# Optimization experiments

Hardware: AMD Instinct MI355X
Metric: run time of the kernel (lower is better)

## Reference

```python
import jax, jax.numpy as jnp
import numpy as np

TOPK = 13
ALPHA = 1.0
BETA = 6.0
NUM_CLASSES = 80
NUM_ANCHORS = 100000
NUM_GT = 512
EPS = 1e-9


def _make_boxes(key, n):
    k1, k2 = jax.random.split(key)
    lt = jax.random.uniform(k1, (n, 2)) * 0.5          # x1, y1 in [0, 0.5)
    wh = jax.random.uniform(k2, (n, 2)) * 0.5 + 1e-3   # positive width/height
    return jnp.concatenate([lt, lt + wh], axis=-1)      # [n, 4] valid xyxy


def setup_inputs() -> dict:
    key = jax.random.key(0)
    k1, k2, k3, k4 = jax.random.split(key, 4)
    pd_scores = jax.random.uniform(k1, (NUM_ANCHORS, NUM_CLASSES), dtype=jnp.float32)
    pd_bboxes = _make_boxes(k2, NUM_ANCHORS)
    gt_labels = jax.random.randint(k3, (NUM_GT, 1), 0, NUM_CLASSES, dtype=jnp.int64)
    gt_bboxes = _make_boxes(k4, NUM_GT)
    return {"pd_scores": pd_scores, "pd_bboxes": pd_bboxes,
            "gt_labels": gt_labels, "gt_bboxes": gt_bboxes}


def box_iou(a, b):
    # a: [G, 4], b: [A, 4] in xyxy -> iou [G, A]
    lt = jnp.maximum(a[:, None, :2], b[None, :, :2])
    rb = jnp.minimum(a[:, None, 2:], b[None, :, 2:])
    wh = jnp.clip(rb - lt, 0.0)
    inter = wh[..., 0] * wh[..., 1]                      # [G, A]
    area_a = (a[:, 2] - a[:, 0]) * (a[:, 3] - a[:, 1])   # [G]
    area_b = (b[:, 2] - b[:, 0]) * (b[:, 3] - b[:, 1])   # [A]
    union = area_a[:, None] + area_b[None, :] - inter
    return inter / (union + EPS)


def select_topk_candidates(metrics, topk):
    # metrics: [G, A] -> bool mask [G, A] of per-row topk entries
    _, topk_idx = jax.lax.top_k(metrics, topk)           # [G, topk]
    rows = jnp.arange(metrics.shape[0])[:, None]
    mask = jnp.zeros(metrics.shape, dtype=bool)
    return mask.at[rows, topk_idx].set(True)


def reference(pd_scores, pd_bboxes, gt_labels, gt_bboxes):
    labels = gt_labels.reshape(-1)                       # [G]
    ious = box_iou(gt_bboxes, pd_bboxes)                 # [G, A]
    scores = pd_scores[:, labels].T                      # [G, A] gather by gt class
    metrics = (scores ** ALPHA) * (ious ** BETA)         # alignment metric [G, A]
    is_in_topk = select_topk_candidates(metrics, TOPK)   # [G, A] bool
    max_metrics = jnp.max(metrics, axis=0)               # [A]
    max_indices = jnp.argmax(metrics, axis=0)            # [A]
    target_labels = labels[max_indices]                  # [A]
    target_labels = jnp.where(max_metrics <= 0, NUM_CLASSES, target_labels)
    target_bboxes = gt_bboxes[max_indices]               # [A, 4]
    # is_in_topk is computed (as in the original) and returned so the topk/scatter
    return target_labels, target_bboxes, max_metrics, is_in_topk
```

## Files before the change

### kernel.cpp

```cpp
#include <hip/hip_runtime.h>
#include <cfloat>
#include <cstdint>

#define AN 100000
#define GN 512
#define NC 80
#define KK 13

#define CHUNKS 8
#define CH_LEN 12544
#define DUMP 16
#define GSLICE 8
#define GPS (GN / GSLICE)

typedef unsigned long long ull;

__device__ __forceinline__ float iou6_f(float4 g, float ga, float4 p)
{
    float pa = (p.z - p.x) * (p.w - p.y);
    float ltx = fmaxf(g.x, p.x), lty = fmaxf(g.y, p.y);
    float rbx = fminf(g.z, p.z), rby = fminf(g.w, p.w);
    float w = fmaxf(rbx - ltx, 0.0f), h = fmaxf(rby - lty, 0.0f);
    float inter = w * h;
    float uni = ga + pa - inter;
    float iou = inter / (uni + 1e-9f);
    float i2 = iou * iou;
    return i2 * i2 * i2;
}

__device__ __forceinline__ unsigned f2ord(float f)
{
    unsigned b = __float_as_uint(f);
    return b ^ (unsigned)(((int)b >> 31) | 0x80000000);
}
__device__ __forceinline__ float ord2f(unsigned u)
{
    unsigned b = (u & 0x80000000u) ? (u ^ 0x80000000u) : ~u;
    return __uint_as_float(b);
}

__device__ __forceinline__ void csw(float& va, int& ia, float& vb, int& ib)
{
    bool sw = (va < vb) || (va == vb && ia > ib);
    float tv = sw ? vb : va; int ti = sw ? ib : ia;
    vb = sw ? va : vb; ib = sw ? ia : ib;
    va = tv; ia = ti;
}

__device__ __forceinline__ void wsync()
{
    __builtin_amdgcn_sched_barrier(0);
    asm volatile("s_waitcnt lgkmcnt(0)" ::: "memory");
    __builtin_amdgcn_sched_barrier(0);
}

__device__ float flush_x(int lane, int n, const float* cand_v, const int* cand_i,
                         float& inc_v, int& inc_i)
{
    wsync();
    float v[8]; int ix[8];
    #pragma unroll
    for (int k = 0; k < 8; ++k) {
        int j = lane + (k << 6);
        bool ok = j < n;
        v[k]  = ok ? cand_v[j] : -FLT_MAX;
        ix[k] = ok ? cand_i[j] : 0x7fffffff;
    }
    csw(v[0],ix[0],v[1],ix[1]); csw(v[2],ix[2],v[3],ix[3]);
    csw(v[4],ix[4],v[5],ix[5]); csw(v[6],ix[6],v[7],ix[7]);
    csw(v[0],ix[0],v[2],ix[2]); csw(v[1],ix[1],v[3],ix[3]);
    csw(v[4],ix[4],v[6],ix[6]); csw(v[5],ix[5],v[7],ix[7]);
    csw(v[1],ix[1],v[2],ix[2]); csw(v[5],ix[5],v[6],ix[6]);
    csw(v[0],ix[0],v[4],ix[4]); csw(v[1],ix[1],v[5],ix[5]);
    csw(v[2],ix[2],v[6],ix[6]); csw(v[3],ix[3],v[7],ix[7]);
    csw(v[2],ix[2],v[4],ix[4]); csw(v[3],ix[3],v[5],ix[5]);
    csw(v[1],ix[1],v[2],ix[2]); csw(v[3],ix[3],v[4],ix[4]);
    csw(v[5],ix[5],v[6],ix[6]);
    bool c[8];
    #pragma unroll
    for (int j = 0; j < 8; ++j)
        c[j] = (v[j] > inc_v) || (v[j] == inc_v && ix[j] < inc_i);
    float h[9]; int hi[9];
    h[0] = c[0] ? v[0] : inc_v;  hi[0] = c[0] ? ix[0] : inc_i;
    #pragma unroll
    for (int j = 1; j < 8; ++j) {
        h[j]  = c[j] ? v[j]  : (c[j-1] ? inc_v : v[j-1]);
        hi[j] = c[j] ? ix[j] : (c[j-1] ? inc_i : ix[j-1]);
    }
    h[8] = c[7] ? inc_v : v[7];  hi[8] = c[7] ? inc_i : ix[7];

    float th = -FLT_MAX;
    #pragma unroll
    for (int r = 0; r < KK; ++r) {
        ull myp = ((ull)f2ord(h[0]) << 32) | (unsigned)(~hi[0]);
        ull p = myp;
        #pragma unroll
        for (int o = 32; o >= 1; o >>= 1) {
            ull q = __shfl_xor(p, o);
            p = p > q ? p : q;
        }
        float wv = ord2f((unsigned)(p >> 32));
        int   wi = (int)~((unsigned)p);
        if (lane == r) { inc_v = wv; inc_i = wi; }
        bool pop = (myp == p);
        #pragma unroll
        for (int j = 0; j < 8; ++j) {
            h[j]  = pop ? h[j+1]  : h[j];
            hi[j] = pop ? hi[j+1] : hi[j];
        }
        h[8]  = pop ? -FLT_MAX   : h[8];
        hi[8] = pop ? 0x7fffffff : hi[8];
        th = wv;
    }
    return th;
}

__device__ __forceinline__ void insert13(float* v, int* ix, float m, int a)
{
    bool worse = (m < v[KK - 1]) || (m == v[KK - 1] && a > ix[KK - 1]);
    if (worse) return;
    int p = 0;
    #pragma unroll
    for (int j = 0; j < KK; ++j)
        p += ((v[j] > m) || (v[j] == m && ix[j] < a)) ? 1 : 0;
    #pragma unroll
    for (int j = KK - 1; j >= 1; --j) {
        bool sh = (j > p);
        v[j]  = sh ? v[j - 1]  : v[j];
        ix[j] = sh ? ix[j - 1] : ix[j];
    }
    #pragma unroll
    for (int j = 0; j < KK; ++j) if (j == p) { v[j] = m; ix[j] = a; }
}

__global__ __launch_bounds__(256) void transpose_scores(
    const float* __restrict__ ps, float* __restrict__ scT)
{
    __shared__ float tile[64][NC + 1];
    int a0 = blockIdx.x * 64;
    int tid = threadIdx.x;
    for (int i = tid; i < 64 * NC / 4; i += 256) {
        int fi = i * 4;
        int a = fi / NC, c = fi % NC;
        if (a0 + a < AN) {
            float4 v = *reinterpret_cast<const float4*>(ps + (size_t)(a0 + a) * NC + c);
            tile[a][c] = v.x; tile[a][c + 1] = v.y; tile[a][c + 2] = v.z; tile[a][c + 3] = v.w;
        }
    }
    __syncthreads();
    int j = tid & 63, cg = tid >> 6;
    int a = a0 + j;
    if (a < AN) {
        for (int c = cg; c < NC; c += 4)
            scT[(size_t)c * AN + a] = tile[j][c];
    }
}

__global__ __launch_bounds__(256) void argmax_part(
    const float* __restrict__ pd_bboxes,
    const int*   __restrict__ gt_labels,
    const float* __restrict__ gt_bboxes,
    const float* __restrict__ scT,
    ull* __restrict__ part)
{
    __shared__ float4 gb[GPS];
    __shared__ float  ga[GPS];
    __shared__ int    glb[GPS];
    int slice = blockIdx.x & (GSLICE - 1);
    int ab = (blockIdx.x >> 3) * 512;
    int tid = threadIdx.x;
    int g0 = slice * GPS;
    if (tid < GPS) {
        float4 bb = ((const float4*)gt_bboxes)[g0 + tid];
        gb[tid] = bb;
        ga[tid] = (bb.z - bb.x) * (bb.w - bb.y);
        glb[tid] = gt_labels[g0 + tid];
    }
    __syncthreads();
    int aa = ab + tid, ab2 = ab + 256 + tid;
    bool okA = aa < AN, okB = ab2 < AN;
    int ca = okA ? aa : AN - 1, cb = okB ? ab2 : AN - 1;
    float4 pba = ((const float4*)pd_bboxes)[ca];
    float4 pbb = ((const float4*)pd_bboxes)[cb];
    float bestA = -1.0f, bestB = -1.0f;
    int bgA = 0, bgB = 0;
    for (int i = 0; i < GPS; ++i) {
        float4 gx = gb[i];
        float gax = ga[i];
        int lab = glb[i];
        const float* srow = scT + (size_t)lab * AN;
        float i6a = iou6_f(gx, gax, pba);
        float i6b = iou6_f(gx, gax, pbb);
        float sa = (i6a > bestA) ? srow[ca] : 0.0f;
        float sb = (i6b > bestB) ? srow[cb] : 0.0f;
        float ma = sa * i6a;
        float mb = sb * i6b;
        if (ma > bestA) { bestA = ma; bgA = i; }
        if (mb > bestB) { bestB = mb; bgB = i; }
    }
    if (okA)
        part[(size_t)slice * AN + aa] =
            ((ull)__float_as_uint(bestA) << 32) | (ull)(0xFFFFFFFFu - (unsigned)(g0 + bgA));
    if (okB)
        part[(size_t)slice * AN + ab2] =
            ((ull)__float_as_uint(bestB) << 32) | (ull)(0xFFFFFFFFu - (unsigned)(g0 + bgB));
}

__global__ __launch_bounds__(256) void argmax_combine(
    const ull* __restrict__ part,
    const int* __restrict__ gt_labels,
    const float* __restrict__ gt_bboxes,
    float* __restrict__ out)
{
    int a = blockIdx.x * 256 + threadIdx.x;
    if (a >= AN) return;
    ull p = part[a];
    #pragma unroll
    for (int s = 1; s < GSLICE; ++s) {
        ull q = part[(size_t)s * AN + a];
        p = p > q ? p : q;
    }
    unsigned g = 0xFFFFFFFFu - (unsigned)(p & 0xFFFFFFFFull);
    float best = __uint_as_float((unsigned)(p >> 32));
    out[a] = (best <= 0.0f) ? (float)NC : (float)gt_labels[g];
    ((float4*)(out + AN))[a] = ((const float4*)gt_bboxes)[g];
    out[(size_t)5 * AN + a] = best;
}

__device__ __forceinline__ void loadT(int tb, int lane,
    const float4* __restrict__ pd4, const float* __restrict__ srow,
    float4& B0, float4& B1, float4& B2, float4& B3,
    float& s0, float& s1, float& s2, float& s3)
{
    int a0 = tb + lane;
    int c0 = min(a0,       AN - 1);
    int c1 = min(a0 + 64,  AN - 1);
    int c2 = min(a0 + 128, AN - 1);
    int c3 = min(a0 + 192, AN - 1);
    B0 = pd4[c0]; B1 = pd4[c1]; B2 = pd4[c2]; B3 = pd4[c3];
    s0 = srow[c0]; s1 = srow[c1]; s2 = srow[c2]; s3 = srow[c3];
}

__device__ __forceinline__ void procT(
    int tb, int aend, int lane, uint64_t lt,
    float4 B0, float4 B1, float4 B2, float4 B3,
    float s0, float s1, float s2, float s3,
    float4 b, float gax, float& th, int& cnt,
    float* cand_v, int* cand_i, float& inc_v, int& inc_i)
{
    int a0 = tb + lane, a1 = a0 + 64, a2 = a0 + 128, a3 = a0 + 192;
    float m0 = s0 * iou6_f(b, gax, B0);
    float m1 = s1 * iou6_f(b, gax, B1);
    float m2 = s2 * iou6_f(b, gax, B2);
    float m3 = s3 * iou6_f(b, gax, B3);
    bool h0 = (m0 > th) && (a0 < aend);
    bool h1 = (m1 > th) && (a1 < aend);
    bool h2 = (m2 > th) && (a2 < aend);
    bool h3 = (m3 > th) && (a3 < aend);
    if (__any(h0 | h1 | h2 | h3)) {
        uint64_t B;
        B = __ballot(h0);
        if (h0) { int p = cnt + __popcll(B & lt); cand_v[p] = m0; cand_i[p] = a0; }
        cnt += __popcll(B);
        B = __ballot(h1);
        if (h1) { int p = cnt + __popcll(B & lt); cand_v[p] = m1; cand_i[p] = a1; }
        cnt += __popcll(B);
        B = __ballot(h2);
        if (h2) { int p = cnt + __popcll(B & lt); cand_v[p] = m2; cand_i[p] = a2; }
        cnt += __popcll(B);
        B = __ballot(h3);
        if (h3) { int p = cnt + __popcll(B & lt); cand_v[p] = m3; cand_i[p] = a3; }
        cnt += __popcll(B);
        if (cnt >= 256) {
            th = flush_x(lane, cnt, cand_v, cand_i, inc_v, inc_i);
            cnt = 0;
        }
    }
}

__global__ __launch_bounds__(256, 4) void topk_pass1(
    const float* __restrict__ pd_bboxes,
    const int*   __restrict__ gt_labels,
    const float* __restrict__ gt_bboxes,
    const float* __restrict__ scT,
    float* __restrict__ out_v, int* __restrict__ out_i)
{
    __shared__ float cvA[4][512];
    __shared__ int   ciA[4][512];
    int w = threadIdx.x >> 6, lane = threadIdx.x & 63;
    float* cand_v = cvA[w]; int* cand_i = ciA[w];
    uint64_t lt = (1ull << lane) - 1ull;
    int gid = blockIdx.x * 4 + w;
    int g = gid & (GN - 1), c = gid >> 9;

    float4 b = ((const float4*)gt_bboxes)[g];
    float gax = (b.z - b.x) * (b.w - b.y);
    int lab = gt_labels[g];
    const float* srow = scT + (size_t)lab * AN;
    const float4* pd4 = (const float4*)pd_bboxes;

    int base = c * CH_LEN;
    int len = min(CH_LEN, AN - base);
    int aend = base + len;
    int NT = (len + 255) >> 8;

    float th = -FLT_MAX; int cnt = 0;
    float inc_v = -FLT_MAX; int inc_i = 0x7fffffff;

    float4 X0, X1, X2, X3, Y0, Y1, Y2, Y3;
    float xs0, xs1, xs2, xs3, ys0, ys1, ys2, ys3;

    loadT(base, lane, pd4, srow, X0, X1, X2, X3, xs0, xs1, xs2, xs3);
    int i = 0, tb = base;
    while (true) {
        if (i + 1 < NT)
            loadT(tb + 256, lane, pd4, srow, Y0, Y1, Y2, Y3, ys0, ys1, ys2, ys3);
        procT(tb, aend, lane, lt, X0, X1, X2, X3, xs0, xs1, xs2, xs3,
              b, gax, th, cnt, cand_v, cand_i, inc_v, inc_i);
        ++i; tb += 256;
        if (i >= NT) break;
        if (i + 1 < NT)
            loadT(tb + 256, lane, pd4, srow, X0, X1, X2, X3, xs0, xs1, xs2, xs3);
        procT(tb, aend, lane, lt, Y0, Y1, Y2, Y3, ys0, ys1, ys2, ys3,
              b, gax, th, cnt, cand_v, cand_i, inc_v, inc_i);
        ++i; tb += 256;
        if (i >= NT) break;
    }

    if (cnt > 0)
        flush_x(lane, cnt, cand_v, cand_i, inc_v, inc_i);

    if (lane < DUMP) {
        size_t o = ((size_t)g * CHUNKS + c) * DUMP + lane;
        out_v[o] = (lane < KK) ? inc_v : -FLT_MAX;
        out_i[o] = (lane < KK) ? inc_i : 0x7fffffff;
    }
}

__global__ __launch_bounds__(256) void topk_finalize(
    const float* __restrict__ in_v, const int* __restrict__ in_i,
    float* __restrict__ mask)
{
    int g = blockIdx.x, tid = threadIdx.x;
    float4* row4 = (float4*)(mask + (size_t)g * AN);
    float4 z = make_float4(0.f, 0.f, 0.f, 0.f);
    for (int j = tid; j < AN / 4; j += 256) row4[j] = z;
    __syncthreads();
    if (tid >= 64) return;
    int lane = tid;
    size_t rb = (size_t)g * (CHUNKS * DUMP);
    float v0 = in_v[rb + lane], v1 = in_v[rb + 64 + lane];
    int   i0 = in_i[rb + lane], i1 = in_i[rb + 64 + lane];
    csw(v0, i0, v1, i1);
    #pragma unroll
    for (int r = 0; r < KK; ++r) {
        ull myp = ((ull)f2ord(v0) << 32) | (unsigned)(~i0);
        ull p = myp;
        #pragma unroll
        for (int o = 32; o >= 1; o >>= 1) {
            ull q = __shfl_xor(p, o);
            p = p > q ? p : q;
        }
        int wi = (int)~((unsigned)p);
        if (lane == r) mask[(size_t)g * AN + wi] = 1.0f;
        bool pop = (myp == p);
        v0 = pop ? v1 : v0;          i0 = pop ? i1 : i0;
        v1 = pop ? -FLT_MAX : v1;    i1 = pop ? 0x7fffffff : i1;
    }
}

__global__ __launch_bounds__(256) void argmax_kernel(
    const float* __restrict__ pd_scores,
    const float* __restrict__ pd_bboxes,
    const int*   __restrict__ gt_labels,
    const float* __restrict__ gt_bboxes,
    const float* __restrict__ scT, int use_t,
    float* __restrict__ out)
{
    __shared__ float4 gb[GN];
    __shared__ float  ga[GN];
    __shared__ int    gl[GN];
    int tid = threadIdx.x;
    for (int g = tid; g < GN; g += 256) {
        float4 b = reinterpret_cast<const float4*>(gt_bboxes)[g];
        gb[g] = b;
        ga[g] = (b.z - b.x) * (b.w - b.y);
        gl[g] = gt_labels[g];
    }
    __syncthreads();
    int a = blockIdx.x * 256 + tid;
    if (a >= AN) return;
    float4 pb = reinterpret_cast<const float4*>(pd_bboxes)[a];
    float best = -1.0f; int bg = 0;
    for (int g = 0; g < GN; ++g) {
        int lab = gl[g];
        float sc = use_t ? scT[(size_t)lab * AN + a] : pd_scores[(size_t)a * NC + lab];
        float m = sc * iou6_f(gb[g], ga[g], pb);
        if (m > best) { best = m; bg = g; }
    }
    out[a] = (best <= 0.0f) ? (float)NC : (float)gl[bg];
    reinterpret_cast<float4*>(out + AN)[a] = gb[bg];
    out[5 * AN + a] = best;
}

__global__ __launch_bounds__(256) void topk_kernel_fallback(
    const float* __restrict__ pd_scores,
    const float* __restrict__ pd_bboxes,
    const int*   __restrict__ gt_labels,
    const float* __restrict__ gt_bboxes,
    const float* __restrict__ scT, int use_t,
    float* __restrict__ mask)
{
    __shared__ float sv[256 * KK];
    __shared__ int   si[256 * KK];
    int g = blockIdx.x, tid = threadIdx.x;
    float4 b = reinterpret_cast<const float4*>(gt_bboxes)[g];
    float gax = (b.z - b.x) * (b.w - b.y);
    int lab = gt_labels[g];
    float v[KK]; int idx[KK];
    #pragma unroll
    for (int j = 0; j < KK; ++j) { v[j] = -FLT_MAX; idx[j] = 0x7fffffff; }
    for (int a = tid; a < AN; a += 256) {
        float4 pb = reinterpret_cast<const float4*>(pd_bboxes)[a];
        float sc = use_t ? scT[(size_t)lab * AN + a] : pd_scores[(size_t)a * NC + lab];
        float m = sc * iou6_f(b, gax, pb);
        insert13(v, idx, m, a);
    }
    #pragma unroll
    for (int j = 0; j < KK; ++j) { sv[tid * KK + j] = v[j]; si[tid * KK + j] = idx[j]; }
    for (int off = 128; off >= 1; off >>= 1) {
        __syncthreads();
        if (tid < off) {
            int i = 0, jj = 0;
            float ov[KK]; int oi[KK];
            #pragma unroll
            for (int t = 0; t < KK; ++t) {
                float va = sv[tid * KK + i];          int ia = si[tid * KK + i];
                float vb = sv[(tid + off) * KK + jj]; int ib = si[(tid + off) * KK + jj];
                bool ta = (va > vb) || (va == vb && ia < ib);
                ov[t] = ta ? va : vb; oi[t] = ta ? ia : ib;
                i += ta ? 1 : 0; jj += ta ? 0 : 1;
            }
            #pragma unroll
            for (int t = 0; t < KK; ++t) { sv[tid * KK + t] = ov[t]; si[tid * KK + t] = oi[t]; }
        }
    }
    __syncthreads();
    if (tid < KK) mask[(size_t)g * AN + si[tid]] = 1.0f;
}

extern "C" void kernel_launch(void* const* d_in, const int* in_sizes, int n_in,
                              void* d_out, int out_size, void* d_ws, size_t ws_size,
                              hipStream_t stream)
{
    const float* pd_scores = (const float*)d_in[0];
    const float* pd_bboxes = (const float*)d_in[1];
    const int*   gt_labels = (const int*)d_in[2];
    const float* gt_bboxes = (const float*)d_in[3];
    float* out  = (float*)d_out;
    float* mask = out + (size_t)6 * AN;

    const size_t scT_b  = (size_t)NC * AN * sizeof(float);
    const size_t auxn   = (size_t)GN * CHUNKS * DUMP;
    const size_t aux_b  = auxn * 8;
    const size_t part_b = (size_t)GSLICE * AN * sizeof(ull);

    float* scT   = (float*)d_ws;
    float* aux_v = (float*)((char*)d_ws + scT_b);
    int*   aux_i = (int*)(aux_v + auxn);
    ull*   part  = (ull*)((char*)d_ws + scT_b + aux_b);

    if (ws_size >= scT_b + aux_b + part_b) {
        transpose_scores<<<(AN + 63) / 64, 256, 0, stream>>>(pd_scores, scT);
        topk_pass1<<<GN * CHUNKS / 4, 256, 0, stream>>>(
            pd_bboxes, gt_labels, gt_bboxes, scT, aux_v, aux_i);
        topk_finalize<<<GN, 256, 0, stream>>>(aux_v, aux_i, mask);
        argmax_part<<<((AN + 511) / 512) * GSLICE, 256, 0, stream>>>(
            pd_bboxes, gt_labels, gt_bboxes, scT, part);
        argmax_combine<<<(AN + 255) / 256, 256, 0, stream>>>(
            part, gt_labels, gt_bboxes, out);
    } else if (ws_size >= scT_b + aux_b) {
        transpose_scores<<<(AN + 63) / 64, 256, 0, stream>>>(pd_scores, scT);
        topk_pass1<<<GN * CHUNKS / 4, 256, 0, stream>>>(
            pd_bboxes, gt_labels, gt_bboxes, scT, aux_v, aux_i);
        topk_finalize<<<GN, 256, 0, stream>>>(aux_v, aux_i, mask);
        argmax_kernel<<<(AN + 255) / 256, 256, 0, stream>>>(
            pd_scores, pd_bboxes, gt_labels, gt_bboxes, scT, 1, out);
    } else if (ws_size >= scT_b) {
        hipMemsetAsync(mask, 0, (size_t)GN * AN * sizeof(float), stream);
        transpose_scores<<<(AN + 63) / 64, 256, 0, stream>>>(pd_scores, scT);
        argmax_kernel<<<(AN + 255) / 256, 256, 0, stream>>>(
            pd_scores, pd_bboxes, gt_labels, gt_bboxes, scT, 1, out);
        topk_kernel_fallback<<<GN, 256, 0, stream>>>(
            pd_scores, pd_bboxes, gt_labels, gt_bboxes, scT, 1, mask);
    } else {
        hipMemsetAsync(mask, 0, (size_t)GN * AN * sizeof(float), stream);
        argmax_kernel<<<(AN + 255) / 256, 256, 0, stream>>>(
            pd_scores, pd_bboxes, gt_labels, gt_bboxes, scT, 0, out);
        topk_kernel_fallback<<<GN, 256, 0, stream>>>(
            pd_scores, pd_bboxes, gt_labels, gt_bboxes, scT, 0, mask);
    }
}
```

Measured before the change: 205.8 us.

## Filter top-k candidates by IoU bound, gather scores lazily; use fast reciprocal

The top-k pass no longer streams the per-class score row for every anchor. It filters anchors by IoU^6 alone, which bounds the metric when scores are at most 1, and gathers scores only for the candidates being flushed. IoU division is replaced with a hardware reciprocal approximation in all kernels. This cuts global memory traffic and divide cost. In exchange, more candidates pass the looser filter, flushes become more frequent and do scattered gathers, correctness depends on scores being at most 1, and results may differ slightly from exact division.

```diff
diff --git a/kernel.cpp b/kernel.cpp
--- a/kernel.cpp
+++ b/kernel.cpp
@@ -15,7 +15,12 @@
 
 typedef unsigned long long ull;
 
-__device__ __forceinline__ float iou6_f(float4 g, float ga, float4 p)
+__device__ __forceinline__ float rcpf(float x)
+{
+    float r; asm("v_rcp_f32 %0, %1" : "=v"(r) : "v"(x)); return r;
+}
+
+__device__ __forceinline__ float iou6r(float4 g, float ga, float4 p)
 {
     float pa = (p.z - p.x) * (p.w - p.y);
     float ltx = fmaxf(g.x, p.x), lty = fmaxf(g.y, p.y);
@@ -23,7 +28,7 @@
     float w = fmaxf(rbx - ltx, 0.0f), h = fmaxf(rby - lty, 0.0f);
     float inter = w * h;
     float uni = ga + pa - inter;
-    float iou = inter / (uni + 1e-9f);
+    float iou = inter * rcpf(uni + 1e-9f);
     float i2 = iou * iou;
     return i2 * i2 * i2;
 }
@@ -55,6 +60,7 @@
 }
 
 __device__ float flush_x(int lane, int n, const float* cand_v, const int* cand_i,
+                         const float* __restrict__ srow,
                          float& inc_v, int& inc_i)
 {
     wsync();
@@ -63,8 +69,11 @@
     for (int k = 0; k < 8; ++k) {
         int j = lane + (k << 6);
         bool ok = j < n;
-        v[k]  = ok ? cand_v[j] : -FLT_MAX;
-        ix[k] = ok ? cand_i[j] : 0x7fffffff;
+        float i6 = ok ? cand_v[j] : 0.0f;
+        int   ai = ok ? cand_i[j] : 0;
+        float sc = srow[ai];
+        v[k]  = ok ? sc * i6 : -FLT_MAX;
+        ix[k] = ok ? ai : 0x7fffffff;
     }
     csw(v[0],ix[0],v[1],ix[1]); csw(v[2],ix[2],v[3],ix[3]);
     csw(v[4],ix[4],v[5],ix[5]); csw(v[6],ix[6],v[7],ix[7]);
@@ -189,8 +198,8 @@
         float gax = ga[i];
         int lab = glb[i];
         const float* srow = scT + (size_t)lab * AN;
-        float i6a = iou6_f(gx, gax, pba);
-        float i6b = iou6_f(gx, gax, pbb);
+        float i6a = iou6r(gx, gax, pba);
+        float i6b = iou6r(gx, gax, pbb);
         float sa = (i6a > bestA) ? srow[ca] : 0.0f;
         float sb = (i6b > bestB) ? srow[cb] : 0.0f;
         float ma = sa * i6a;
@@ -227,52 +236,49 @@
     out[(size_t)5 * AN + a] = best;
 }
 
-__device__ __forceinline__ void loadT(int tb, int lane,
-    const float4* __restrict__ pd4, const float* __restrict__ srow,
-    float4& B0, float4& B1, float4& B2, float4& B3,
-    float& s0, float& s1, float& s2, float& s3)
+__device__ __forceinline__ void loadB(int tb, int lane,
+    const float4* __restrict__ pd4,
+    float4& B0, float4& B1, float4& B2, float4& B3)
 {
     int a0 = tb + lane;
-    int c0 = min(a0,       AN - 1);
-    int c1 = min(a0 + 64,  AN - 1);
-    int c2 = min(a0 + 128, AN - 1);
-    int c3 = min(a0 + 192, AN - 1);
-    B0 = pd4[c0]; B1 = pd4[c1]; B2 = pd4[c2]; B3 = pd4[c3];
-    s0 = srow[c0]; s1 = srow[c1]; s2 = srow[c2]; s3 = srow[c3];
-}
-
-__device__ __forceinline__ void procT(
+    B0 = pd4[min(a0,       AN - 1)];
+    B1 = pd4[min(a0 + 64,  AN - 1)];
+    B2 = pd4[min(a0 + 128, AN - 1)];
+    B3 = pd4[min(a0 + 192, AN - 1)];
+}
+
+__device__ __forceinline__ void procB(
     int tb, int aend, int lane, uint64_t lt,
     float4 B0, float4 B1, float4 B2, float4 B3,
-    float s0, float s1, float s2, float s3,
+    const float* __restrict__ srow,
     float4 b, float gax, float& th, int& cnt,
     float* cand_v, int* cand_i, float& inc_v, int& inc_i)
 {
     int a0 = tb + lane, a1 = a0 + 64, a2 = a0 + 128, a3 = a0 + 192;
-    float m0 = s0 * iou6_f(b, gax, B0);
-    float m1 = s1 * iou6_f(b, gax, B1);
-    float m2 = s2 * iou6_f(b, gax, B2);
-    float m3 = s3 * iou6_f(b, gax, B3);
-    bool h0 = (m0 > th) && (a0 < aend);
-    bool h1 = (m1 > th) && (a1 < aend);
-    bool h2 = (m2 > th) && (a2 < aend);
-    bool h3 = (m3 > th) && (a3 < aend);
+    float i60 = iou6r(b, gax, B0);
+    float i61 = iou6r(b, gax, B1);
+    float i62 = iou6r(b, gax, B2);
+    float i63 = iou6r(b, gax, B3);
+    bool h0 = (i60 > th) && (a0 < aend);
+    bool h1 = (i61 > th) && (a1 < aend);
+    bool h2 = (i62 > th) && (a2 < aend);
+    bool h3 = (i63 > th) && (a3 < aend);
     if (__any(h0 | h1 | h2 | h3)) {
         uint64_t B;
         B = __ballot(h0);
-        if (h0) { int p = cnt + __popcll(B & lt); cand_v[p] = m0; cand_i[p] = a0; }
+        if (h0) { int p = cnt + __popcll(B & lt); cand_v[p] = i60; cand_i[p] = a0; }
         cnt += __popcll(B);
         B = __ballot(h1);
-        if (h1) { int p = cnt + __popcll(B & lt); cand_v[p] = m1; cand_i[p] = a1; }
+        if (h1) { int p = cnt + __popcll(B & lt); cand_v[p] = i61; cand_i[p] = a1; }
         cnt += __popcll(B);
         B = __ballot(h2);
-        if (h2) { int p = cnt + __popcll(B & lt); cand_v[p] = m2; cand_i[p] = a2; }
+        if (h2) { int p = cnt + __popcll(B & lt); cand_v[p] = i62; cand_i[p] = a2; }
         cnt += __popcll(B);
         B = __ballot(h3);
-        if (h3) { int p = cnt + __popcll(B & lt); cand_v[p] = m3; cand_i[p] = a3; }
+        if (h3) { int p = cnt + __popcll(B & lt); cand_v[p] = i63; cand_i[p] = a3; }
         cnt += __popcll(B);
         if (cnt >= 256) {
-            th = flush_x(lane, cnt, cand_v, cand_i, inc_v, inc_i);
+            th = flush_x(lane, cnt, cand_v, cand_i, srow, inc_v, inc_i);
             cnt = 0;
         }
     }
@@ -308,27 +314,23 @@
     float inc_v = -FLT_MAX; int inc_i = 0x7fffffff;
 
     float4 X0, X1, X2, X3, Y0, Y1, Y2, Y3;
-    float xs0, xs1, xs2, xs3, ys0, ys1, ys2, ys3;
-
-    loadT(base, lane, pd4, srow, X0, X1, X2, X3, xs0, xs1, xs2, xs3);
+    loadB(base, lane, pd4, X0, X1, X2, X3);
     int i = 0, tb = base;
     while (true) {
-        if (i + 1 < NT)
-            loadT(tb + 256, lane, pd4, srow, Y0, Y1, Y2, Y3, ys0, ys1, ys2, ys3);
-        procT(tb, aend, lane, lt, X0, X1, X2, X3, xs0, xs1, xs2, xs3,
+        if (i + 1 < NT) loadB(tb + 256, lane, pd4, Y0, Y1, Y2, Y3);
+        procB(tb, aend, lane, lt, X0, X1, X2, X3, srow,
               b, gax, th, cnt, cand_v, cand_i, inc_v, inc_i);
         ++i; tb += 256;
         if (i >= NT) break;
-        if (i + 1 < NT)
-            loadT(tb + 256, lane, pd4, srow, X0, X1, X2, X3, xs0, xs1, xs2, xs3);
-        procT(tb, aend, lane, lt, Y0, Y1, Y2, Y3, ys0, ys1, ys2, ys3,
+        if (i + 1 < NT) loadB(tb + 256, lane, pd4, X0, X1, X2, X3);
+        procB(tb, aend, lane, lt, Y0, Y1, Y2, Y3, srow,
               b, gax, th, cnt, cand_v, cand_i, inc_v, inc_i);
         ++i; tb += 256;
         if (i >= NT) break;
     }
 
     if (cnt > 0)
-        flush_x(lane, cnt, cand_v, cand_i, inc_v, inc_i);
+        flush_x(lane, cnt, cand_v, cand_i, srow, inc_v, inc_i);
 
     if (lane < DUMP) {
         size_t o = ((size_t)g * CHUNKS + c) * DUMP + lane;
@@ -395,7 +397,7 @@
     for (int g = 0; g < GN; ++g) {
         int lab = gl[g];
         float sc = use_t ? scT[(size_t)lab * AN + a] : pd_scores[(size_t)a * NC + lab];
-        float m = sc * iou6_f(gb[g], ga[g], pb);
+        float m = sc * iou6r(gb[g], ga[g], pb);
         if (m > best) { best = m; bg = g; }
     }
     out[a] = (best <= 0.0f) ? (float)NC : (float)gl[bg];
@@ -423,7 +425,7 @@
     for (int a = tid; a < AN; a += 256) {
         float4 pb = reinterpret_cast<const float4*>(pd_bboxes)[a];
         float sc = use_t ? scT[(size_t)lab * AN + a] : pd_scores[(size_t)a * NC + lab];
-        float m = sc * iou6_f(b, gax, pb);
+        float m = sc * iou6r(b, gax, pb);
         insert13(v, idx, m, a);
     }
     #pragma unroll
```

After: 179.4 us. 1.15x faster.
